# Kernel tuning notes

Measured on AMD Instinct MI355X. Metric: run time of the kernel, lower is better.

## Reference

```python
import jax, jax.numpy as jnp
import numpy as np

B, L, D, H = 4, 1024, 1024, 16
HD = D // H  # head_dim = 64


def setup_inputs() -> dict:
    key = jax.random.key(0)
    k1, k2, k3, k4 = jax.random.split(key, 4)
    x = jax.random.normal(k1, (B, L, D), dtype=jnp.float32)
    # causal mask: positions where mask == 0 are filled with -inf
    mask = jnp.tril(jnp.ones((L, L), dtype=bool))[None, None, :, :]  # [1,1,L,L]
    w_qkv = jax.random.normal(k2, (D, 3 * D), dtype=jnp.float32) * (D ** -0.5)
    w_out = jax.random.normal(k3, (D, D), dtype=jnp.float32) * (D ** -0.5)
    rel_pos_bias = jax.random.normal(k4, (H, L, L), dtype=jnp.float32) * 0.02
    return {"x": x, "mask": mask, "w_qkv": w_qkv, "w_out": w_out,
            "rel_pos_bias": rel_pos_bias}


def reference(x, mask, w_qkv, w_out, rel_pos_bias):
    b, l, d = x.shape
    scale = HD ** -0.5
    qkv = (x @ w_qkv).reshape(b, l, 3, H, HD)          # [B,L,3,H,hd]
    q, k, v = qkv[:, :, 0], qkv[:, :, 1], qkv[:, :, 2]  # each [B,L,H,hd]
    # scores: [B,H,Lq,Lk]
    scores = jnp.einsum('bqhd,bkhd->bhqk', q, k) * scale
    scores = scores + rel_pos_bias[None, :, :l, :l]
    scores = jnp.where(mask, scores, -jnp.inf)
    attn = jax.nn.softmax(scores, axis=-1)  # dropout is identity in eval
    out = jnp.einsum('bhqk,bkhd->bqhd', attn, v).reshape(b, l, d)
    return out @ w_out
```

## Files before the change

### kernel.cpp

```cpp
#include <hip/hip_runtime.h>
#include <hip/hip_bf16.h>
#include <math.h>

#define B_  4
#define L_  1024
#define D_  1024
#define H_  16
#define HD_ 64
#define SCALE 0.125f
#define LOG2E 1.44269504f
#define SCALE_L2E (0.125f * 1.44269504f)
#define NEG_BIG -3.0e38f

typedef __bf16 bf16x8 __attribute__((ext_vector_type(8)));
typedef float  f32x4  __attribute__((ext_vector_type(4)));

__device__ __forceinline__ float b2f(unsigned short u) {
    union { unsigned int i; float f; } x; x.i = ((unsigned)u) << 16; return x.f;
}
__device__ __forceinline__ unsigned short f2b(float f) {
    __hip_bfloat16 h = __float2bfloat16(f);
    return *reinterpret_cast<unsigned short*>(&h);
}
__device__ __forceinline__ void gl_lds16(const void* g, void* l) {
    __builtin_amdgcn_global_load_lds(
        (const __attribute__((address_space(1))) void*)g,
        (__attribute__((address_space(3))) void*)l, 16, 0, 0);
}

__global__ __launch_bounds__(256) void prep_kernel(
    const float* __restrict__ x, const float* __restrict__ w_qkv,
    const float* __restrict__ w_out, unsigned short* __restrict__ xb,
    unsigned short* __restrict__ wqkvT, unsigned short* __restrict__ woutT)
{
    const int bid = blockIdx.x;
    if (bid < 4096) {
        int i = (bid * 256 + threadIdx.x) * 4;
        float4 v = *(const float4*)&x[i];
        ushort4 o = make_ushort4(f2b(v.x), f2b(v.y), f2b(v.z), f2b(v.w));
        *(ushort4*)&xb[i] = o;
        return;
    }
    __shared__ float tile[32][33];
    const float* w; unsigned short* wt; int N, n0, k0;
    if (bid < 7168) {
        int b2 = bid - 4096;
        w = w_qkv; wt = wqkvT; N = 3072;
        n0 = (b2 % 96) * 32; k0 = (b2 / 96) * 32;
    } else {
        int b3 = bid - 7168;
        w = w_out; wt = woutT; N = 1024;
        n0 = (b3 % 32) * 32; k0 = (b3 / 32) * 32;
    }
    const int tx = threadIdx.x & 31, ty = threadIdx.x >> 5;
#pragma unroll
    for (int i = 0; i < 4; i++) {
        int kk = ty + i * 8;
        tile[kk][tx] = w[(size_t)(k0 + kk) * N + n0 + tx];
    }
    __syncthreads();
#pragma unroll
    for (int i = 0; i < 4; i++) {
        int nn = ty + i * 8;
        wt[(size_t)(n0 + nn) * 1024 + k0 + tx] = f2b(tile[tx][nn]);
    }
}

__device__ __forceinline__ void gemm_core64(
    const unsigned short* __restrict__ A, const unsigned short* __restrict__ Bt,
    unsigned short* As, unsigned short* Bs,
    int m0, int n0, int wave, int lane, int wm, int wn,
    f32x4 acc[4][4])
{
    const int srow = lane >> 2, spos = lane & 3;
    const int sc   = spos ^ ((srow >> 1) & 3);
    const int mlane = lane & 15, chunk = lane >> 4;
    const int foff  = mlane * 32 + (chunk ^ ((mlane >> 1) & 3)) * 8;

    for (int k0 = 0; k0 < 1024; k0 += 64) {
#pragma unroll
        for (int p = 0; p < 2; p++) {
            const int kp = k0 + p * 32;
            unsigned short* Ap = As + p * 4096;
            unsigned short* Bp = Bs + p * 4096;
#pragma unroll
            for (int t = 0; t < 2; t++) {
                int rb = wave * 32 + t * 16;
                int r  = rb + srow;
                gl_lds16(&A [(size_t)(m0 + r) * 1024 + kp + sc * 8], &Ap[rb * 32]);
                gl_lds16(&Bt[(size_t)(n0 + r) * 1024 + kp + sc * 8], &Bp[rb * 32]);
            }
        }
        __syncthreads();
#pragma unroll
        for (int p = 0; p < 2; p++) {
            const unsigned short* Ap = As + p * 4096;
            const unsigned short* Bp = Bs + p * 4096;
            bf16x8 af[4], bfr[4];
#pragma unroll
            for (int i = 0; i < 4; i++) {
                af[i]  = *(const bf16x8*)&Ap[(wm * 64 + i * 16) * 32 + foff];
                bfr[i] = *(const bf16x8*)&Bp[(wn * 64 + i * 16) * 32 + foff];
            }
#pragma unroll
            for (int i = 0; i < 4; i++)
#pragma unroll
                for (int j = 0; j < 4; j++)
                    acc[i][j] = __builtin_amdgcn_mfma_f32_16x16x32_bf16(
                        bfr[i], af[j], acc[i][j], 0, 0, 0);
        }
        __syncthreads();
    }
}

__global__ __launch_bounds__(256) void qkv_gemm_kernel(
    const unsigned short* __restrict__ A, const unsigned short* __restrict__ Bt,
    unsigned short* __restrict__ qb, unsigned short* __restrict__ kb,
    unsigned short* __restrict__ vtb)
{
    __shared__ unsigned short As[2 * 128 * 32];
    __shared__ unsigned short Bs[2 * 128 * 32];
    const int tid  = threadIdx.x;
    const int wave = tid >> 6, lane = tid & 63;
    const int quad = lane >> 4, l16 = lane & 15;
    const int wm = wave >> 1, wn = wave & 1;
    const int lin = blockIdx.x;
    const int sw  = (lin & 7) * 96 + (lin >> 3);
    const int m0 = (sw / 24) * 128, n0 = (sw % 24) * 128;
    f32x4 acc[4][4] = {};
    gemm_core64(A, Bt, As, Bs, m0, n0, wave, lane, wm, wn, acc);

    const int s = n0 >> 10;
#pragma unroll
    for (int i = 0; i < 4; i++) {
        int n_base = n0 + wn * 64 + i * 16 + quad * 4;
        int h = (n_base >> 6) & 15, hd0 = n_base & 63;
#pragma unroll
        for (int j = 0; j < 4; j++) {
            int m = m0 + wm * 64 + j * 16 + l16;
            int b = m >> 10, l = m & 1023;
            if (s == 2) {
#pragma unroll
                for (int r = 0; r < 4; r++)
                    vtb[((size_t)((b * 16 + h) * 64 + hd0 + r)) * 1024 + l] =
                        f2b(acc[i][j][r]);
            } else {
                unsigned short* dst = (s == 0) ? qb : kb;
                unsigned short tmp[4];
#pragma unroll
                for (int r = 0; r < 4; r++) tmp[r] = f2b(acc[i][j][r]);
                *(ushort4*)&dst[(((size_t)(b * 16 + h) * 1024 + l) << 6) + hd0] =
                    *(ushort4*)tmp;
            }
        }
    }
}

__global__ __launch_bounds__(256) void out_gemm_kernel(
    const unsigned short* __restrict__ A, const unsigned short* __restrict__ Bt,
    float* __restrict__ out)
{
    __shared__ unsigned short As[2 * 128 * 32];
    __shared__ unsigned short Bs[2 * 64 * 32];
    const int tid  = threadIdx.x;
    const int wave = tid >> 6, lane = tid & 63;
    const int quad = lane >> 4, l16 = lane & 15;
    const int srow = lane >> 2, spos = lane & 3;
    const int sc   = spos ^ ((srow >> 1) & 3);
    const int mlane = lane & 15, chunk = lane >> 4;
    const int foff  = mlane * 32 + (chunk ^ ((mlane >> 1) & 3)) * 8;
    const int lin = blockIdx.x;
    const int sw  = (lin & 7) * 64 + (lin >> 3);
    const int m0 = (sw >> 4) * 128, n0 = (sw & 15) * 64;
    f32x4 acc[4][2] = {};

    for (int k0 = 0; k0 < 1024; k0 += 64) {
#pragma unroll
        for (int p = 0; p < 2; p++) {
            const int kp = k0 + p * 32;
            unsigned short* Ap = As + p * 4096;
            unsigned short* Bp = Bs + p * 2048;
#pragma unroll
            for (int t = 0; t < 2; t++) {
                int rb = wave * 32 + t * 16;
                gl_lds16(&A[(size_t)(m0 + rb + srow) * 1024 + kp + sc * 8], &Ap[rb * 32]);
            }
            {
                int rb = wave * 16;
                gl_lds16(&Bt[(size_t)(n0 + rb + srow) * 1024 + kp + sc * 8], &Bp[rb * 32]);
            }
        }
        __syncthreads();
#pragma unroll
        for (int p = 0; p < 2; p++) {
            const unsigned short* Ap = As + p * 4096;
            const unsigned short* Bp = Bs + p * 2048;
            bf16x8 af[2], bfr[4];
#pragma unroll
            for (int i = 0; i < 2; i++)
                af[i]  = *(const bf16x8*)&Ap[(wave * 32 + i * 16) * 32 + foff];
#pragma unroll
            for (int j = 0; j < 4; j++)
                bfr[j] = *(const bf16x8*)&Bp[(j * 16) * 32 + foff];
#pragma unroll
            for (int jn = 0; jn < 4; jn++)
#pragma unroll
                for (int im = 0; im < 2; im++)
                    acc[jn][im] = __builtin_amdgcn_mfma_f32_16x16x32_bf16(
                        bfr[jn], af[im], acc[jn][im], 0, 0, 0);
        }
        __syncthreads();
    }
#pragma unroll
    for (int jn = 0; jn < 4; jn++) {
        int n_base = n0 + jn * 16 + quad * 4;
#pragma unroll
        for (int im = 0; im < 2; im++) {
            int m = m0 + wave * 32 + im * 16 + l16;
            float4 o = make_float4(acc[jn][im][0], acc[jn][im][1],
                                   acc[jn][im][2], acc[jn][im][3]);
            *(float4*)&out[(size_t)m * 1024 + n_base] = o;
        }
    }
}

__global__ __launch_bounds__(256, 4) void attn_mfma_kernel(
    const unsigned short* __restrict__ qb, const unsigned short* __restrict__ kb,
    const unsigned short* __restrict__ vtb, const float* __restrict__ bias,
    unsigned short* __restrict__ ob)
{
    __shared__ unsigned short Ks [2 * 64 * 72];
    __shared__ unsigned short Vts[2 * 64 * 72];

    const int tid  = threadIdx.x;
    const int wave = tid >> 6, lane = tid & 63;
    const int quad = lane >> 4, l16 = lane & 15;
    const int bh = blockIdx.x, b = bh >> 4, h = bh & 15;
    const int yk = blockIdx.y & 3, seg = blockIdx.y >> 2;
    const int qt = (seg == 0) ? 15 - yk : (seg == 1) ? yk
                 : (seg == 2) ? 11 - yk : yk + 4;
    const int q0 = qt * 64;
    const int srow = tid >> 3, scol = (tid & 7) * 8;
    const size_t qkv_base = (size_t)bh * (1024 * 64);

    const int qrow  = q0 + wave * 16;
    const int qlane = qrow + l16;

    bf16x8 a0 = *(const bf16x8*)&qb[qkv_base + (size_t)(qrow + l16) * 64 + quad * 8];
    bf16x8 a1 = *(const bf16x8*)&qb[qkv_base + (size_t)(qrow + l16) * 64 + 32 + quad * 8];

    uint4 kpre0 = *(const uint4*)&kb [qkv_base + (size_t)srow * 64 + scol];
    uint4 kpre1 = *(const uint4*)&kb [qkv_base + (size_t)(srow + 32) * 64 + scol];
    uint4 vpre0 = *(const uint4*)&vtb[qkv_base + (size_t)srow * 1024 + scol];
    uint4 vpre1 = *(const uint4*)&vtb[qkv_base + (size_t)(srow + 32) * 1024 + scol];

    const float* bias_row = &bias[((size_t)h * 1024 + qlane) * 1024];

    float bA[16], bB[16];
#pragma unroll
    for (int nt = 0; nt < 4; nt++) {
        float4 b4 = *(const float4*)&bias_row[nt * 16 + quad * 4];
        bA[nt * 4 + 0] = b4.x * LOG2E; bA[nt * 4 + 1] = b4.y * LOG2E;
        bA[nt * 4 + 2] = b4.z * LOG2E; bA[nt * 4 + 3] = b4.w * LOG2E;
    }

    float lr = 0.f;
    f32x4 O[4] = {};

    *(uint4*)&Ks [srow * 72 + scol]        = kpre0;
    *(uint4*)&Ks [(srow + 32) * 72 + scol] = kpre1;
    *(uint4*)&Vts[srow * 72 + scol]        = vpre0;
    *(uint4*)&Vts[(srow + 32) * 72 + scol] = vpre1;
    __syncthreads();

    auto tile = [&](int kt, float* bc, float* bn) {
        const bool pf = (kt < qt);
        if (pf) {
            const int kn = (kt + 1) * 64;
            kpre0 = *(const uint4*)&kb [qkv_base + (size_t)(kn + srow) * 64 + scol];
            kpre1 = *(const uint4*)&kb [qkv_base + (size_t)(kn + srow + 32) * 64 + scol];
            vpre0 = *(const uint4*)&vtb[qkv_base + (size_t)srow * 1024 + kn + scol];
            vpre1 = *(const uint4*)&vtb[qkv_base + (size_t)(srow + 32) * 1024 + kn + scol];
#pragma unroll
            for (int nt = 0; nt < 4; nt++) {
                float4 b4 = *(const float4*)&bias_row[kn + nt * 16 + quad * 4];
                bn[nt * 4 + 0] = b4.x * LOG2E; bn[nt * 4 + 1] = b4.y * LOG2E;
                bn[nt * 4 + 2] = b4.z * LOG2E; bn[nt * 4 + 3] = b4.w * LOG2E;
            }
        }
        const unsigned short* Kc = &Ks [(kt & 1) * 4608];
        const unsigned short* Vc = &Vts[(kt & 1) * 4608];
        f32x4 sacc[4] = {};
        __builtin_amdgcn_s_setprio(1);
#pragma unroll
        for (int nt = 0; nt < 4; nt++) {
            bf16x8 k0 = *(const bf16x8*)&Kc[(nt * 16 + l16) * 72 + quad * 8];
            bf16x8 k1 = *(const bf16x8*)&Kc[(nt * 16 + l16) * 72 + 32 + quad * 8];
            sacc[nt] = __builtin_amdgcn_mfma_f32_16x16x32_bf16(k0, a0, sacc[nt], 0, 0, 0);
            sacc[nt] = __builtin_amdgcn_mfma_f32_16x16x32_bf16(k1, a1, sacc[nt], 0, 0, 0);
        }
        __builtin_amdgcn_s_setprio(0);
        const bool dg = (kt == qt);
        const int kb0 = kt * 64 + quad * 4;
        unsigned int pk[4][2];
#pragma unroll
        for (int nt = 0; nt < 4; nt++) {
            float ps[4];
#pragma unroll
            for (int r = 0; r < 4; r++) {
                float v = fmaf(sacc[nt][r], SCALE_L2E, bc[nt * 4 + r]);
                if (dg && (kb0 + nt * 16 + r) > qlane) v = NEG_BIG;
                ps[r] = exp2f(v);
            }
            lr += (ps[0] + ps[1]) + (ps[2] + ps[3]);
            asm("v_cvt_pk_bf16_f32 %0, %1, %2"
                : "=v"(pk[nt][0]) : "v"(ps[0]), "v"(ps[1]));
            asm("v_cvt_pk_bf16_f32 %0, %1, %2"
                : "=v"(pk[nt][1]) : "v"(ps[2]), "v"(ps[3]));
        }
        unsigned int pa[4], pb[4];
#pragma unroll
        for (int i = 0; i < 2; i++) {
            unsigned int xa = pk[0][i], xb = pk[1][i];
            asm("v_permlane32_swap_b32 %0, %1" : "+v"(xa), "+v"(xb));
            asm("v_permlane16_swap_b32 %0, %1" : "+v"(xa), "+v"(xb));
            pa[i] = xa; pa[2 + i] = xb;
            unsigned int xc = pk[2][i], xd = pk[3][i];
            asm("v_permlane32_swap_b32 %0, %1" : "+v"(xc), "+v"(xd));
            asm("v_permlane16_swap_b32 %0, %1" : "+v"(xc), "+v"(xd));
            pb[i] = xc; pb[2 + i] = xd;
        }
        union { unsigned int u[4]; bf16x8 v; } U0, U1;
        U0.u[0] = pa[0]; U0.u[1] = pa[1]; U0.u[2] = pa[2]; U0.u[3] = pa[3];
        U1.u[0] = pb[0]; U1.u[1] = pb[1]; U1.u[2] = pb[2]; U1.u[3] = pb[3];
        bf16x8 p0 = U0.v, p1 = U1.v;
        __builtin_amdgcn_s_setprio(1);
#pragma unroll
        for (int dt = 0; dt < 4; dt++) {
            bf16x8 v0 = *(const bf16x8*)&Vc[(dt * 16 + l16) * 72 + quad * 8];
            bf16x8 v1 = *(const bf16x8*)&Vc[(dt * 16 + l16) * 72 + 32 + quad * 8];
            O[dt] = __builtin_amdgcn_mfma_f32_16x16x32_bf16(p0, v0, O[dt], 0, 0, 0);
            O[dt] = __builtin_amdgcn_mfma_f32_16x16x32_bf16(p1, v1, O[dt], 0, 0, 0);
        }
        __builtin_amdgcn_s_setprio(0);
        if (pf) {
            unsigned short* Kn = &Ks [((kt + 1) & 1) * 4608];
            unsigned short* Vn = &Vts[((kt + 1) & 1) * 4608];
            *(uint4*)&Kn[srow * 72 + scol]        = kpre0;
            *(uint4*)&Kn[(srow + 32) * 72 + scol] = kpre1;
            *(uint4*)&Vn[srow * 72 + scol]        = vpre0;
            *(uint4*)&Vn[(srow + 32) * 72 + scol] = vpre1;
        }
        __syncthreads();
    };

    for (int kt = 0; kt <= qt; kt += 2) {
        tile(kt, bA, bB);
        if (kt + 1 <= qt) tile(kt + 1, bB, bA);
    }

    lr += __shfl_xor(lr, 16);
    lr += __shfl_xor(lr, 32);

#pragma unroll
    for (int r = 0; r < 4; r++) {
        float s = __shfl(lr, quad * 4 + r);
        float inv = 1.0f / s;
        int qgr = qrow + quad * 4 + r;
#pragma unroll
        for (int dt = 0; dt < 4; dt++)
            ob[((size_t)(b * 1024 + qgr)) * 1024 + h * 64 + dt * 16 + l16] =
                f2b(O[dt][r] * inv);
    }
}


extern "C" void kernel_launch(void* const* d_in, const int* in_sizes, int n_in,
                              void* d_out, int out_size, void* d_ws, size_t ws_size,
                              hipStream_t stream) {
    const float* x     = (const float*)d_in[0];
    const float* w_qkv = (const float*)d_in[2];
    const float* w_out = (const float*)d_in[3];
    const float* bias  = (const float*)d_in[4];
    float* out = (float*)d_out;

    char* ws = (char*)d_ws;
    unsigned short* xb     = (unsigned short*)ws;              ws += (size_t)4096 * 1024 * 2;
    unsigned short* wqkvT  = (unsigned short*)ws;              ws += (size_t)3072 * 1024 * 2;
    unsigned short* woutT  = (unsigned short*)ws;              ws += (size_t)1024 * 1024 * 2;
    unsigned short* qb     = (unsigned short*)ws;              ws += (size_t)4096 * 1024 * 2;
    unsigned short* kb     = (unsigned short*)ws;              ws += (size_t)4096 * 1024 * 2;
    unsigned short* vtb    = (unsigned short*)ws;              ws += (size_t)4096 * 1024 * 2;
    unsigned short* ab     = (unsigned short*)ws;

    prep_kernel<<<8192, 256, 0, stream>>>(x, w_qkv, w_out, xb, wqkvT, woutT);
    qkv_gemm_kernel<<<768, 256, 0, stream>>>(xb, wqkvT, qb, kb, vtb);
    attn_mfma_kernel<<<dim3(64, 16), 256, 0, stream>>>(qb, kb, vtb, bias, ab);
    out_gemm_kernel<<<512, 256, 0, stream>>>(ab, woutT, out);
}
```

Measured before the change: 212.3 us.

## Use 128-row query tiles with 8 waves sharing each K/V tile

The attention kernel now runs 512-thread blocks covering 128 query rows, with 8 waves sharing each K/V LDS tile that is loaded one row per thread. This halves the K/V global loads and LDS fills per query row. Waves in the lower 64 rows skip the final tile. Query tiles are ordered in pairs so causal work is balanced across the 8 y-blocks. The cost is fewer blocks (512 instead of 1024), some idle waves on the last tile, and more register and occupancy pressure under the 512-thread launch bound.

```diff
diff --git a/kernel.cpp b/kernel.cpp
--- a/kernel.cpp
+++ b/kernel.cpp
@@ -224,7 +224,7 @@
     }
 }
 
-__global__ __launch_bounds__(256, 4) void attn_mfma_kernel(
+__global__ __launch_bounds__(512, 4) void attn_mfma_kernel(
     const unsigned short* __restrict__ qb, const unsigned short* __restrict__ kb,
     const unsigned short* __restrict__ vtb, const float* __restrict__ bias,
     unsigned short* __restrict__ ob)
@@ -236,10 +236,11 @@
     const int wave = tid >> 6, lane = tid & 63;
     const int quad = lane >> 4, l16 = lane & 15;
     const int bh = blockIdx.x, b = bh >> 4, h = bh & 15;
-    const int yk = blockIdx.y & 3, seg = blockIdx.y >> 2;
-    const int qt = (seg == 0) ? 15 - yk : (seg == 1) ? yk
-                 : (seg == 2) ? 11 - yk : yk + 4;
-    const int q0 = qt * 64;
+    const int y = blockIdx.y;
+    const int j = (y < 4) ? y : 11 - y;
+    const int q0 = j * 128;
+    const int ktmax = 2 * j + 1;
+    const int qtw = 2 * j + (wave >> 2);
     const int srow = tid >> 3, scol = (tid & 7) * 8;
     const size_t qkv_base = (size_t)bh * (1024 * 64);
 
@@ -249,10 +250,8 @@
     bf16x8 a0 = *(const bf16x8*)&qb[qkv_base + (size_t)(qrow + l16) * 64 + quad * 8];
     bf16x8 a1 = *(const bf16x8*)&qb[qkv_base + (size_t)(qrow + l16) * 64 + 32 + quad * 8];
 
-    uint4 kpre0 = *(const uint4*)&kb [qkv_base + (size_t)srow * 64 + scol];
-    uint4 kpre1 = *(const uint4*)&kb [qkv_base + (size_t)(srow + 32) * 64 + scol];
-    uint4 vpre0 = *(const uint4*)&vtb[qkv_base + (size_t)srow * 1024 + scol];
-    uint4 vpre1 = *(const uint4*)&vtb[qkv_base + (size_t)(srow + 32) * 1024 + scol];
+    uint4 kpre = *(const uint4*)&kb [qkv_base + (size_t)srow * 64 + scol];
+    uint4 vpre = *(const uint4*)&vtb[qkv_base + (size_t)srow * 1024 + scol];
 
     const float* bias_row = &bias[((size_t)h * 1024 + qlane) * 1024];
 
@@ -267,20 +266,16 @@
     float lr = 0.f;
     f32x4 O[4] = {};
 
-    *(uint4*)&Ks [srow * 72 + scol]        = kpre0;
-    *(uint4*)&Ks [(srow + 32) * 72 + scol] = kpre1;
-    *(uint4*)&Vts[srow * 72 + scol]        = vpre0;
-    *(uint4*)&Vts[(srow + 32) * 72 + scol] = vpre1;
+    *(uint4*)&Ks [srow * 72 + scol] = kpre;
+    *(uint4*)&Vts[srow * 72 + scol] = vpre;
     __syncthreads();
 
     auto tile = [&](int kt, float* bc, float* bn) {
-        const bool pf = (kt < qt);
+        const bool pf = (kt < ktmax);
         if (pf) {
             const int kn = (kt + 1) * 64;
-            kpre0 = *(const uint4*)&kb [qkv_base + (size_t)(kn + srow) * 64 + scol];
-            kpre1 = *(const uint4*)&kb [qkv_base + (size_t)(kn + srow + 32) * 64 + scol];
-            vpre0 = *(const uint4*)&vtb[qkv_base + (size_t)srow * 1024 + kn + scol];
-            vpre1 = *(const uint4*)&vtb[qkv_base + (size_t)(srow + 32) * 1024 + kn + scol];
+            kpre = *(const uint4*)&kb [qkv_base + (size_t)(kn + srow) * 64 + scol];
+            vpre = *(const uint4*)&vtb[qkv_base + (size_t)srow * 1024 + kn + scol];
 #pragma unroll
             for (int nt = 0; nt < 4; nt++) {
                 float4 b4 = *(const float4*)&bias_row[kn + nt * 16 + quad * 4];
@@ -288,75 +283,75 @@
                 bn[nt * 4 + 2] = b4.z * LOG2E; bn[nt * 4 + 3] = b4.w * LOG2E;
             }
         }
-        const unsigned short* Kc = &Ks [(kt & 1) * 4608];
-        const unsigned short* Vc = &Vts[(kt & 1) * 4608];
-        f32x4 sacc[4] = {};
-        __builtin_amdgcn_s_setprio(1);
-#pragma unroll
-        for (int nt = 0; nt < 4; nt++) {
-            bf16x8 k0 = *(const bf16x8*)&Kc[(nt * 16 + l16) * 72 + quad * 8];
-            bf16x8 k1 = *(const bf16x8*)&Kc[(nt * 16 + l16) * 72 + 32 + quad * 8];
-            sacc[nt] = __builtin_amdgcn_mfma_f32_16x16x32_bf16(k0, a0, sacc[nt], 0, 0, 0);
-            sacc[nt] = __builtin_amdgcn_mfma_f32_16x16x32_bf16(k1, a1, sacc[nt], 0, 0, 0);
-        }
-        __builtin_amdgcn_s_setprio(0);
-        const bool dg = (kt == qt);
-        const int kb0 = kt * 64 + quad * 4;
-        unsigned int pk[4][2];
-#pragma unroll
-        for (int nt = 0; nt < 4; nt++) {
-            float ps[4];
-#pragma unroll
-            for (int r = 0; r < 4; r++) {
-                float v = fmaf(sacc[nt][r], SCALE_L2E, bc[nt * 4 + r]);
-                if (dg && (kb0 + nt * 16 + r) > qlane) v = NEG_BIG;
-                ps[r] = exp2f(v);
-            }
-            lr += (ps[0] + ps[1]) + (ps[2] + ps[3]);
-            asm("v_cvt_pk_bf16_f32 %0, %1, %2"
-                : "=v"(pk[nt][0]) : "v"(ps[0]), "v"(ps[1]));
-            asm("v_cvt_pk_bf16_f32 %0, %1, %2"
-                : "=v"(pk[nt][1]) : "v"(ps[2]), "v"(ps[3]));
-        }
-        unsigned int pa[4], pb[4];
-#pragma unroll
-        for (int i = 0; i < 2; i++) {
-            unsigned int xa = pk[0][i], xb = pk[1][i];
-            asm("v_permlane32_swap_b32 %0, %1" : "+v"(xa), "+v"(xb));
-            asm("v_permlane16_swap_b32 %0, %1" : "+v"(xa), "+v"(xb));
-            pa[i] = xa; pa[2 + i] = xb;
-            unsigned int xc = pk[2][i], xd = pk[3][i];
-            asm("v_permlane32_swap_b32 %0, %1" : "+v"(xc), "+v"(xd));
-            asm("v_permlane16_swap_b32 %0, %1" : "+v"(xc), "+v"(xd));
-            pb[i] = xc; pb[2 + i] = xd;
-        }
-        union { unsigned int u[4]; bf16x8 v; } U0, U1;
-        U0.u[0] = pa[0]; U0.u[1] = pa[1]; U0.u[2] = pa[2]; U0.u[3] = pa[3];
-        U1.u[0] = pb[0]; U1.u[1] = pb[1]; U1.u[2] = pb[2]; U1.u[3] = pb[3];
-        bf16x8 p0 = U0.v, p1 = U1.v;
-        __builtin_amdgcn_s_setprio(1);
-#pragma unroll
-        for (int dt = 0; dt < 4; dt++) {
-            bf16x8 v0 = *(const bf16x8*)&Vc[(dt * 16 + l16) * 72 + quad * 8];
-            bf16x8 v1 = *(const bf16x8*)&Vc[(dt * 16 + l16) * 72 + 32 + quad * 8];
-            O[dt] = __builtin_amdgcn_mfma_f32_16x16x32_bf16(p0, v0, O[dt], 0, 0, 0);
-            O[dt] = __builtin_amdgcn_mfma_f32_16x16x32_bf16(p1, v1, O[dt], 0, 0, 0);
-        }
-        __builtin_amdgcn_s_setprio(0);
+        if (kt <= qtw) {
+            const unsigned short* Kc = &Ks [(kt & 1) * 4608];
+            const unsigned short* Vc = &Vts[(kt & 1) * 4608];
+            f32x4 sacc[4] = {};
+            __builtin_amdgcn_s_setprio(1);
+#pragma unroll
+            for (int nt = 0; nt < 4; nt++) {
+                bf16x8 k0 = *(const bf16x8*)&Kc[(nt * 16 + l16) * 72 + quad * 8];
+                bf16x8 k1 = *(const bf16x8*)&Kc[(nt * 16 + l16) * 72 + 32 + quad * 8];
+                sacc[nt] = __builtin_amdgcn_mfma_f32_16x16x32_bf16(k0, a0, sacc[nt], 0, 0, 0);
+                sacc[nt] = __builtin_amdgcn_mfma_f32_16x16x32_bf16(k1, a1, sacc[nt], 0, 0, 0);
+            }
+            __builtin_amdgcn_s_setprio(0);
+            const bool dg = (kt == qtw);
+            const int kb0 = kt * 64 + quad * 4;
+            unsigned int pk[4][2];
+#pragma unroll
+            for (int nt = 0; nt < 4; nt++) {
+                float ps[4];
+#pragma unroll
+                for (int r = 0; r < 4; r++) {
+                    float v = fmaf(sacc[nt][r], SCALE_L2E, bc[nt * 4 + r]);
+                    if (dg && (kb0 + nt * 16 + r) > qlane) v = NEG_BIG;
+                    ps[r] = exp2f(v);
+                }
+                lr += (ps[0] + ps[1]) + (ps[2] + ps[3]);
+                asm("v_cvt_pk_bf16_f32 %0, %1, %2"
+                    : "=v"(pk[nt][0]) : "v"(ps[0]), "v"(ps[1]));
+                asm("v_cvt_pk_bf16_f32 %0, %1, %2"
+                    : "=v"(pk[nt][1]) : "v"(ps[2]), "v"(ps[3]));
+            }
+            unsigned int pa[4], pb[4];
+#pragma unroll
+            for (int i = 0; i < 2; i++) {
+                unsigned int xa = pk[0][i], xb = pk[1][i];
+                asm("v_permlane32_swap_b32 %0, %1" : "+v"(xa), "+v"(xb));
+                asm("v_permlane16_swap_b32 %0, %1" : "+v"(xa), "+v"(xb));
+                pa[i] = xa; pa[2 + i] = xb;
+                unsigned int xc = pk[2][i], xd = pk[3][i];
+                asm("v_permlane32_swap_b32 %0, %1" : "+v"(xc), "+v"(xd));
+                asm("v_permlane16_swap_b32 %0, %1" : "+v"(xc), "+v"(xd));
+                pb[i] = xc; pb[2 + i] = xd;
+            }
+            union { unsigned int u[4]; bf16x8 v; } U0, U1;
+            U0.u[0] = pa[0]; U0.u[1] = pa[1]; U0.u[2] = pa[2]; U0.u[3] = pa[3];
+            U1.u[0] = pb[0]; U1.u[1] = pb[1]; U1.u[2] = pb[2]; U1.u[3] = pb[3];
+            bf16x8 p0 = U0.v, p1 = U1.v;
+            __builtin_amdgcn_s_setprio(1);
+#pragma unroll
+            for (int dt = 0; dt < 4; dt++) {
+                bf16x8 v0 = *(const bf16x8*)&Vc[(dt * 16 + l16) * 72 + quad * 8];
+                bf16x8 v1 = *(const bf16x8*)&Vc[(dt * 16 + l16) * 72 + 32 + quad * 8];
+                O[dt] = __builtin_amdgcn_mfma_f32_16x16x32_bf16(p0, v0, O[dt], 0, 0, 0);
+                O[dt] = __builtin_amdgcn_mfma_f32_16x16x32_bf16(p1, v1, O[dt], 0, 0, 0);
+            }
+            __builtin_amdgcn_s_setprio(0);
+        }
         if (pf) {
             unsigned short* Kn = &Ks [((kt + 1) & 1) * 4608];
             unsigned short* Vn = &Vts[((kt + 1) & 1) * 4608];
-            *(uint4*)&Kn[srow * 72 + scol]        = kpre0;
-            *(uint4*)&Kn[(srow + 32) * 72 + scol] = kpre1;
-            *(uint4*)&Vn[srow * 72 + scol]        = vpre0;
-            *(uint4*)&Vn[(srow + 32) * 72 + scol] = vpre1;
+            *(uint4*)&Kn[srow * 72 + scol] = kpre;
+            *(uint4*)&Vn[srow * 72 + scol] = vpre;
         }
         __syncthreads();
     };
 
-    for (int kt = 0; kt <= qt; kt += 2) {
+    for (int kt = 0; kt <= ktmax; kt += 2) {
         tile(kt, bA, bB);
-        if (kt + 1 <= qt) tile(kt + 1, bB, bA);
+        if (kt + 1 <= ktmax) tile(kt + 1, bB, bA);
     }
 
     lr += __shfl_xor(lr, 16);
@@ -395,6 +390,6 @@
 
     prep_kernel<<<8192, 256, 0, stream>>>(x, w_qkv, w_out, xb, wqkvT, woutT);
     qkv_gemm_kernel<<<768, 256, 0, stream>>>(xb, wqkvT, qb, kb, vtb);
-    attn_mfma_kernel<<<dim3(64, 16), 256, 0, stream>>>(qb, kb, vtb, bias, ab);
+    attn_mfma_kernel<<<dim3(64, 8), 512, 0, stream>>>(qb, kb, vtb, bias, ab);
     out_gemm_kernel<<<512, 256, 0, stream>>>(ab, woutT, out);
 }
```

After: 219.1 us. 1.03x slower.

## Reuse 128x128 gemm core for output projection and batch x conversion per thread

Applied to the files above, without the earlier changes.

The output projection GEMM now uses the shared 128x128-tile gemm_core64 routine (2x2 wave layout, 4x4 accumulators) instead of its own 128x64 tile loop. This halves the block count to 256 and raises data reuse per block. The x-to-bf16 conversion in the prep kernel now handles four float4 chunks per thread, cutting the prep grid from 8192 to 5120 blocks. The larger tile risks lower occupancy, and 256 blocks may underfill the GPU.

```diff
diff --git a/kernel.cpp b/kernel.cpp
--- a/kernel.cpp
+++ b/kernel.cpp
@@ -34,21 +34,25 @@
     unsigned short* __restrict__ wqkvT, unsigned short* __restrict__ woutT)
 {
     const int bid = blockIdx.x;
-    if (bid < 4096) {
-        int i = (bid * 256 + threadIdx.x) * 4;
-        float4 v = *(const float4*)&x[i];
-        ushort4 o = make_ushort4(f2b(v.x), f2b(v.y), f2b(v.z), f2b(v.w));
-        *(ushort4*)&xb[i] = o;
+    if (bid < 1024) {
+        int base = bid * 256 + threadIdx.x;
+#pragma unroll
+        for (int v = 0; v < 4; v++) {
+            int i = (base + v * 262144) * 4;
+            float4 f = *(const float4*)&x[i];
+            ushort4 o = make_ushort4(f2b(f.x), f2b(f.y), f2b(f.z), f2b(f.w));
+            *(ushort4*)&xb[i] = o;
+        }
         return;
     }
     __shared__ float tile[32][33];
     const float* w; unsigned short* wt; int N, n0, k0;
-    if (bid < 7168) {
-        int b2 = bid - 4096;
+    if (bid < 4096) {
+        int b2 = bid - 1024;
         w = w_qkv; wt = wqkvT; N = 3072;
         n0 = (b2 % 96) * 32; k0 = (b2 / 96) * 32;
     } else {
-        int b3 = bid - 7168;
+        int b3 = bid - 4096;
         w = w_out; wt = woutT; N = 1024;
         n0 = (b3 % 32) * 32; k0 = (b3 / 32) * 32;
     }
@@ -161,64 +165,25 @@
     float* __restrict__ out)
 {
     __shared__ unsigned short As[2 * 128 * 32];
-    __shared__ unsigned short Bs[2 * 64 * 32];
+    __shared__ unsigned short Bs[2 * 128 * 32];
     const int tid  = threadIdx.x;
     const int wave = tid >> 6, lane = tid & 63;
     const int quad = lane >> 4, l16 = lane & 15;
-    const int srow = lane >> 2, spos = lane & 3;
-    const int sc   = spos ^ ((srow >> 1) & 3);
-    const int mlane = lane & 15, chunk = lane >> 4;
-    const int foff  = mlane * 32 + (chunk ^ ((mlane >> 1) & 3)) * 8;
+    const int wm = wave >> 1, wn = wave & 1;
     const int lin = blockIdx.x;
-    const int sw  = (lin & 7) * 64 + (lin >> 3);
-    const int m0 = (sw >> 4) * 128, n0 = (sw & 15) * 64;
-    f32x4 acc[4][2] = {};
-
-    for (int k0 = 0; k0 < 1024; k0 += 64) {
-#pragma unroll
-        for (int p = 0; p < 2; p++) {
-            const int kp = k0 + p * 32;
-            unsigned short* Ap = As + p * 4096;
-            unsigned short* Bp = Bs + p * 2048;
-#pragma unroll
-            for (int t = 0; t < 2; t++) {
-                int rb = wave * 32 + t * 16;
-                gl_lds16(&A[(size_t)(m0 + rb + srow) * 1024 + kp + sc * 8], &Ap[rb * 32]);
-            }
-            {
-                int rb = wave * 16;
-                gl_lds16(&Bt[(size_t)(n0 + rb + srow) * 1024 + kp + sc * 8], &Bp[rb * 32]);
-            }
-        }
-        __syncthreads();
-#pragma unroll
-        for (int p = 0; p < 2; p++) {
-            const unsigned short* Ap = As + p * 4096;
-            const unsigned short* Bp = Bs + p * 2048;
-            bf16x8 af[2], bfr[4];
-#pragma unroll
-            for (int i = 0; i < 2; i++)
-                af[i]  = *(const bf16x8*)&Ap[(wave * 32 + i * 16) * 32 + foff];
-#pragma unroll
-            for (int j = 0; j < 4; j++)
-                bfr[j] = *(const bf16x8*)&Bp[(j * 16) * 32 + foff];
-#pragma unroll
-            for (int jn = 0; jn < 4; jn++)
-#pragma unroll
-                for (int im = 0; im < 2; im++)
-                    acc[jn][im] = __builtin_amdgcn_mfma_f32_16x16x32_bf16(
-                        bfr[jn], af[im], acc[jn][im], 0, 0, 0);
-        }
-        __syncthreads();
-    }
-#pragma unroll
-    for (int jn = 0; jn < 4; jn++) {
-        int n_base = n0 + jn * 16 + quad * 4;
-#pragma unroll
-        for (int im = 0; im < 2; im++) {
-            int m = m0 + wave * 32 + im * 16 + l16;
-            float4 o = make_float4(acc[jn][im][0], acc[jn][im][1],
-                                   acc[jn][im][2], acc[jn][im][3]);
+    const int sw  = (lin & 7) * 32 + (lin >> 3);
+    const int m0 = (sw >> 3) * 128, n0 = (sw & 7) * 128;
+    f32x4 acc[4][4] = {};
+    gemm_core64(A, Bt, As, Bs, m0, n0, wave, lane, wm, wn, acc);
+
+#pragma unroll
+    for (int i = 0; i < 4; i++) {
+        int n_base = n0 + wn * 64 + i * 16 + quad * 4;
+#pragma unroll
+        for (int j = 0; j < 4; j++) {
+            int m = m0 + wm * 64 + j * 16 + l16;
+            float4 o = make_float4(acc[i][j][0], acc[i][j][1],
+                                   acc[i][j][2], acc[i][j][3]);
             *(float4*)&out[(size_t)m * 1024 + n_base] = o;
         }
     }
@@ -393,8 +358,8 @@
     unsigned short* vtb    = (unsigned short*)ws;              ws += (size_t)4096 * 1024 * 2;
     unsigned short* ab     = (unsigned short*)ws;
 
-    prep_kernel<<<8192, 256, 0, stream>>>(x, w_qkv, w_out, xb, wqkvT, woutT);
+    prep_kernel<<<5120, 256, 0, stream>>>(x, w_qkv, w_out, xb, wqkvT, woutT);
     qkv_gemm_kernel<<<768, 256, 0, stream>>>(xb, wqkvT, qb, kb, vtb);
     attn_mfma_kernel<<<dim3(64, 16), 256, 0, stream>>>(qb, kb, vtb, bias, ab);
-    out_gemm_kernel<<<512, 256, 0, stream>>>(ab, woutT, out);
-}
+    out_gemm_kernel<<<256, 256, 0, stream>>>(ab, woutT, out);
+}
```

Result: slower. 224.7 us (+5.8%).
